# Optimization experiments

Hardware: AMD Instinct MI355X
Metric: run time of the kernel (lower is better)

Reference implementation:

```python
import jax, jax.numpy as jnp
import numpy as np
import math

GROUPS = 32
EPS = 1e-5
N_HEADS = 8  # channels=512 / num_head_channels=64


def group_norm(x, w, b):
    # x: [B, C, T]; GroupNorm over (channels-in-group, T)
    B, C, T = x.shape
    xg = x.reshape(B, GROUPS, C // GROUPS * T)
    mu = xg.mean(axis=-1, keepdims=True)
    var = xg.var(axis=-1, keepdims=True)
    xn = ((xg - mu) * jax.lax.rsqrt(var + EPS)).reshape(B, C, T)
    return xn * w[None, :, None] + b[None, :, None]


def setup_inputs() -> dict:
    key = jax.random.key(0)
    ks = jax.random.split(key, 7)
    C = 512
    return {
        "x": jax.random.normal(ks[0], (8, C, 32, 32), dtype=jnp.float32),
        "norm_w": jax.random.normal(ks[1], (C,), dtype=jnp.float32),
        "norm_b": jax.random.normal(ks[2], (C,), dtype=jnp.float32),
        "qkv_w": jax.random.normal(ks[3], (3 * C, C), dtype=jnp.float32) * 0.02,
        "qkv_b": jax.random.normal(ks[4], (3 * C,), dtype=jnp.float32) * 0.02,
        "proj_w": jax.random.normal(ks[5], (C, C), dtype=jnp.float32) * 0.02,
        "proj_b": jax.random.normal(ks[6], (C,), dtype=jnp.float32) * 0.02,
    }


def reference(x, norm_w, norm_b, qkv_w, qkv_b, proj_w, proj_b):
    b, c, H, W = x.shape
    T = H * W
    xf = x.reshape(b, c, T)
    xn = group_norm(xf, norm_w, norm_b)
    # 1x1 conv1d == channel matmul: [3C, C] x [B, C, T] -> [B, 3C, T]
    qkv = jnp.einsum('oc,bct->bot', qkv_w, xn) + qkv_b[None, :, None]
    ch = c // N_HEADS
    qkv = qkv.reshape(b * N_HEADS, 3 * ch, T)
    q, k, v = qkv[:, :ch], qkv[:, ch:2 * ch], qkv[:, 2 * ch:]
    scale = 1.0 / math.sqrt(math.sqrt(ch))
    # [BH, T, T] score matrix (explicit, as in the original)
    weight = jnp.einsum('bct,bcs->bts', q * scale, k * scale)
    weight = jax.nn.softmax(weight.astype(jnp.float32), axis=-1).astype(qkv.dtype)
    a = jnp.einsum('bts,bcs->bct', weight, v).reshape(b, c, T)
    hout = jnp.einsum('oc,bct->bot', proj_w, a) + proj_b[None, :, None]
    return (xf + hout).reshape(b, c, H, W)
```

## Files before the change

kernel.cpp:

```cpp
#include <hip/hip_runtime.h>
#include <math.h>

typedef float f32x4_t __attribute__((ext_vector_type(4)));
typedef short bf16x8_t __attribute__((ext_vector_type(8)));

#define B_   8
#define C_   512
#define T_   1024
#define NH_  8
#define CH_  64
#define EPSF 1e-5f

#define MFMA16(a, b, c) __builtin_amdgcn_mfma_f32_16x16x32_bf16((a), (b), (c), 0, 0, 0)

__device__ __forceinline__ unsigned short f2bf(float f) {
  union { float f; unsigned u; } v; v.f = f;
  unsigned r = v.u + 0x7FFFu + ((v.u >> 16) & 1u);
  return (unsigned short)(r >> 16);
}

__global__ __launch_bounds__(256) void prep_gn_kernel(
    const float* __restrict__ x, const float* __restrict__ w,
    const float* __restrict__ bvec, unsigned short* __restrict__ xnT,
    const float* __restrict__ qw_f, const float* __restrict__ pw_f,
    unsigned short* __restrict__ qw, unsigned short* __restrict__ pw)
{
  int tid = threadIdx.x;
  if (blockIdx.x >= 256) {
    int idx = (blockIdx.x - 256) * 256 + tid;
    const int N1 = 1536 * 512 / 4;
    const int N2 = 512 * 512 / 4;
    if (idx < N1) {
      float4 v = ((const float4*)qw_f)[idx];
      uint2 o;
      o.x = (unsigned)f2bf(v.x) | ((unsigned)f2bf(v.y) << 16);
      o.y = (unsigned)f2bf(v.z) | ((unsigned)f2bf(v.w) << 16);
      ((uint2*)qw)[idx] = o;
    } else if (idx < N1 + N2) {
      int j = idx - N1;
      float4 v = ((const float4*)pw_f)[j];
      uint2 o;
      o.x = (unsigned)f2bf(v.x) | ((unsigned)f2bf(v.y) << 16);
      o.y = (unsigned)f2bf(v.z) | ((unsigned)f2bf(v.w) << 16);
      ((uint2*)pw)[j] = o;
    }
    return;
  }

  int blk = blockIdx.x;
  int b = blk >> 5, g = blk & 31;
  const float* xp = x + ((size_t)(b * C_ + g * 16)) * T_;
  const int N = 16 * T_;

  float s = 0.f, s2 = 0.f;
  for (int i = tid * 4; i < N; i += 256 * 4) {
    float4 v = *(const float4*)(xp + i);
    s  += v.x + v.y + v.z + v.w;
    s2 += v.x * v.x + v.y * v.y + v.z * v.z + v.w * v.w;
  }
  for (int off = 32; off; off >>= 1) {
    s  += __shfl_down(s,  off, 64);
    s2 += __shfl_down(s2, off, 64);
  }
  __shared__ float rs_[4], r2_[4];
  __shared__ float mu_s, rsig_s;
  int wid = tid >> 6, lane = tid & 63;
  if (lane == 0) { rs_[wid] = s; r2_[wid] = s2; }
  __syncthreads();
  if (tid == 0) {
    float ts = rs_[0] + rs_[1] + rs_[2] + rs_[3];
    float t2 = r2_[0] + r2_[1] + r2_[2] + r2_[3];
    float mu = ts / (float)N;
    float var = t2 / (float)N - mu * mu;
    mu_s = mu;
    rsig_s = rsqrtf(var + EPSF);
  }
  __syncthreads();
  float mu = mu_s, rs = rsig_s;

  float wl[16], bl[16];
  for (int c = 0; c < 16; ++c) { wl[c] = w[g * 16 + c]; bl[c] = bvec[g * 16 + c]; }

  for (int t = tid; t < T_; t += 256) {
    unsigned short buf[16] __attribute__((aligned(16)));
    for (int c = 0; c < 16; ++c) {
      float val = xp[(size_t)c * T_ + t];
      buf[c] = f2bf((val - mu) * rs * wl[c] + bl[c]);
    }
    unsigned short* dst = xnT + ((size_t)b * T_ + t) * C_ + g * 16;
    *(uint4*)dst       = *(uint4*)buf;
    *(uint4*)(dst + 8) = *(uint4*)(buf + 8);
  }
}

__global__ __launch_bounds__(256) void gemm_qkv_kernel(
    const unsigned short* __restrict__ W, const unsigned short* __restrict__ xnT,
    const float* __restrict__ bias,
    unsigned short* __restrict__ q_t, unsigned short* __restrict__ k_t,
    unsigned short* __restrict__ v_c)
{
  int b = blockIdx.z;
  int m0 = blockIdx.y * 128, n0 = blockIdx.x * 128;
  int tid = threadIdx.x;
  int w = tid >> 6, lane = tid & 63, quad = lane >> 4, lr = lane & 15;
  int wm = w >> 1, wn = w & 1;

  __shared__ __align__(16) unsigned short Asl[128][40];
  __shared__ __align__(16) unsigned short Bsl[128][40];

  f32x4_t acc[4][4];
  for (int i = 0; i < 4; ++i)
    for (int j = 0; j < 4; ++j) acc[i][j] = (f32x4_t){0.f, 0.f, 0.f, 0.f};

  const unsigned short* Bbase = xnT + ((size_t)b * T_ + n0) * C_;

  int ur = tid >> 2, uk = (tid & 3) * 8;
  uint4 pa0 = *(const uint4*)&W[(size_t)(m0 + ur) * C_ + uk];
  uint4 pa1 = *(const uint4*)&W[(size_t)(m0 + ur + 64) * C_ + uk];
  uint4 pb0 = *(const uint4*)&Bbase[(size_t)ur * C_ + uk];
  uint4 pb1 = *(const uint4*)&Bbase[(size_t)(ur + 64) * C_ + uk];

  for (int k0 = 0; k0 < C_; k0 += 32) {
    __syncthreads();
    *(uint4*)&Asl[ur][uk]      = pa0;
    *(uint4*)&Asl[ur + 64][uk] = pa1;
    *(uint4*)&Bsl[ur][uk]      = pb0;
    *(uint4*)&Bsl[ur + 64][uk] = pb1;
    if (k0 + 32 < C_) {
      pa0 = *(const uint4*)&W[(size_t)(m0 + ur) * C_ + k0 + 32 + uk];
      pa1 = *(const uint4*)&W[(size_t)(m0 + ur + 64) * C_ + k0 + 32 + uk];
      pb0 = *(const uint4*)&Bbase[(size_t)ur * C_ + k0 + 32 + uk];
      pb1 = *(const uint4*)&Bbase[(size_t)(ur + 64) * C_ + k0 + 32 + uk];
    }
    __syncthreads();
    bf16x8_t af[4], bfv[4];
    for (int i = 0; i < 4; ++i) af[i]  = *(bf16x8_t*)&Asl[wm * 64 + i * 16 + lr][quad * 8];
    for (int j = 0; j < 4; ++j) bfv[j] = *(bf16x8_t*)&Bsl[wn * 64 + j * 16 + lr][quad * 8];
    for (int i = 0; i < 4; ++i)
      for (int j = 0; j < 4; ++j)
        acc[i][j] = MFMA16(af[i], bfv[j], acc[i][j]);
  }

  for (int i = 0; i < 4; ++i) {
    int ob = m0 + wm * 64 + i * 16 + quad * 4;
    int h = ob / 192, r0 = ob % 192;
    for (int j = 0; j < 4; ++j) {
      int t = n0 + wn * 64 + j * 16 + lr;
      if (r0 < 128) {
        unsigned short pk[4] __attribute__((aligned(8)));
      #pragma unroll
        for (int r = 0; r < 4; ++r) pk[r] = f2bf(acc[i][j][r] + bias[ob + r]);
        unsigned short* base = (r0 < 64) ? q_t : k_t;
        int chn = (r0 < 64) ? r0 : r0 - 64;
        *(uint2*)&base[((size_t)(b * NH_ + h) * T_ + t) * CH_ + chn] = *(uint2*)pk;
      } else {
      #pragma unroll
        for (int r = 0; r < 4; ++r) {
          float vv = acc[i][j][r] + bias[ob + r];
          v_c[((size_t)(b * NH_ + h) * CH_ + (r0 - 128 + r)) * T_ + t] = f2bf(vv);
        }
      }
    }
  }
}

__global__ __launch_bounds__(256) void attn_kernel(
    const unsigned short* __restrict__ q_t, const unsigned short* __restrict__ k_t,
    const unsigned short* __restrict__ v_c, unsigned short* __restrict__ a_t)
{
  int t0 = blockIdx.x * 64;
  int bh = blockIdx.y;
  int tid = threadIdx.x;
  int w = tid >> 6, lane = tid & 63, quad = lane >> 4, lr = lane & 15;

  __shared__ __align__(16) unsigned short q_s[64][72];
  __shared__ __align__(16) unsigned short k_s[64][72];
  __shared__ __align__(16) unsigned short v_s[64][72];
  __shared__ __align__(16) unsigned short p_s[64][72];

  int r0 = tid >> 3, c0 = (tid & 7) * 8;
  *(uint4*)&q_s[r0][c0] =
      *(const uint4*)&q_t[((size_t)bh * T_ + t0 + r0) * CH_ + c0];
  *(uint4*)&q_s[r0 + 32][c0] =
      *(const uint4*)&q_t[((size_t)bh * T_ + t0 + r0 + 32) * CH_ + c0];

  uint4 kr0 = *(const uint4*)&k_t[((size_t)bh * T_ + r0) * CH_ + c0];
  uint4 kr1 = *(const uint4*)&k_t[((size_t)bh * T_ + r0 + 32) * CH_ + c0];
  uint4 vr0 = *(const uint4*)&v_c[((size_t)bh * CH_ + r0) * T_ + c0];
  uint4 vr1 = *(const uint4*)&v_c[((size_t)bh * CH_ + r0 + 32) * T_ + c0];

  __syncthreads();
  bf16x8_t aq[2];
  aq[0] = *(bf16x8_t*)&q_s[w * 16 + lr][quad * 8];
  aq[1] = *(bf16x8_t*)&q_s[w * 16 + lr][32 + quad * 8];

  bf16x8_t ones8;
  {
    short ov = (lr == 0) ? (short)0x3F80 : (short)0;
    for (int e = 0; e < 8; ++e) ones8[e] = ov;
  }

  f32x4_t o_acc[4], o_l;
  for (int j = 0; j < 4; ++j) o_acc[j] = (f32x4_t){0.f, 0.f, 0.f, 0.f};
  o_l = (f32x4_t){0.f, 0.f, 0.f, 0.f};

  const float SCL = 0.18033688f;
  const float MSH = 11.541560f;

  for (int s0 = 0; s0 < T_; s0 += 64) {
    __syncthreads();
    *(uint4*)&k_s[r0][c0]      = kr0;
    *(uint4*)&k_s[r0 + 32][c0] = kr1;
    *(uint4*)&v_s[r0][c0]      = vr0;
    *(uint4*)&v_s[r0 + 32][c0] = vr1;
    if (s0 + 64 < T_) {
      kr0 = *(const uint4*)&k_t[((size_t)bh * T_ + s0 + 64 + r0) * CH_ + c0];
      kr1 = *(const uint4*)&k_t[((size_t)bh * T_ + s0 + 96 + r0) * CH_ + c0];
      vr0 = *(const uint4*)&v_c[((size_t)bh * CH_ + r0) * T_ + s0 + 64 + c0];
      vr1 = *(const uint4*)&v_c[((size_t)bh * CH_ + r0 + 32) * T_ + s0 + 64 + c0];
    }
    __syncthreads();

    f32x4_t sc[4];
    for (int j = 0; j < 4; ++j) {
      f32x4_t a2 = (f32x4_t){0.f, 0.f, 0.f, 0.f};
      for (int kk = 0; kk < 2; ++kk) {
        bf16x8_t bk = *(bf16x8_t*)&k_s[j * 16 + lr][kk * 32 + quad * 8];
        a2 = MFMA16(aq[kk], bk, a2);
      }
      sc[j] = a2;
    }

    for (int j = 0; j < 4; ++j)
      for (int r = 0; r < 4; ++r) {
        float p = __builtin_amdgcn_exp2f(sc[j][r] * SCL - MSH);
        union { float f; unsigned u; } cv; cv.f = p;
        p_s[w * 16 + quad * 4 + r][j * 16 + lr] = (unsigned short)(cv.u >> 16);
      }
    bf16x8_t ap[2];
    ap[0] = *(bf16x8_t*)&p_s[w * 16 + lr][quad * 8];
    ap[1] = *(bf16x8_t*)&p_s[w * 16 + lr][32 + quad * 8];

    o_l = MFMA16(ap[0], ones8, o_l);
    o_l = MFMA16(ap[1], ones8, o_l);
    for (int j = 0; j < 4; ++j)
      for (int kk = 0; kk < 2; ++kk) {
        bf16x8_t bv = *(bf16x8_t*)&v_s[j * 16 + lr][kk * 32 + quad * 8];
        o_acc[j] = MFMA16(ap[kk], bv, o_acc[j]);
      }
  }

  float lv[4];
  for (int r = 0; r < 4; ++r) lv[r] = __shfl(o_l[r], lane & 48, 64);
  for (int r = 0; r < 4; ++r) {
    float inv = 1.f / lv[r];
    for (int j = 0; j < 4; ++j)
      q_s[w * 16 + quad * 4 + r][j * 16 + lr] = f2bf(o_acc[j][r] * inv);
  }
  __syncthreads();
  *(uint4*)&a_t[((size_t)bh * T_ + t0 + r0) * CH_ + c0]      = *(uint4*)&q_s[r0][c0];
  *(uint4*)&a_t[((size_t)bh * T_ + t0 + r0 + 32) * CH_ + c0] = *(uint4*)&q_s[r0 + 32][c0];
}

__global__ __launch_bounds__(256) void gemm_proj_kernel(
    const unsigned short* __restrict__ W, const unsigned short* __restrict__ a_t,
    const float* __restrict__ bias, const float* __restrict__ xres,
    float* __restrict__ out)
{
  int b = blockIdx.z;
  int m0 = blockIdx.y * 128, n0 = blockIdx.x * 128;
  int tid = threadIdx.x;
  int w = tid >> 6, lane = tid & 63, quad = lane >> 4, lr = lane & 15;
  int wm = w >> 1, wn = w & 1;

  __shared__ __align__(16) unsigned short Asl[128][40];
  __shared__ __align__(16) unsigned short Bsl[128][40];

  f32x4_t acc[4][4];
  for (int i = 0; i < 4; ++i)
    for (int j = 0; j < 4; ++j) acc[i][j] = (f32x4_t){0.f, 0.f, 0.f, 0.f};

  int ur = tid >> 2, uk = (tid & 3) * 8;
  const unsigned short* Bb0 = a_t + ((size_t)(b * NH_ + 0) * T_ + n0) * CH_;
  uint4 pa0 = *(const uint4*)&W[(size_t)(m0 + ur) * C_ + uk];
  uint4 pa1 = *(const uint4*)&W[(size_t)(m0 + ur + 64) * C_ + uk];
  uint4 pb0 = *(const uint4*)&Bb0[(size_t)ur * CH_ + uk];
  uint4 pb1 = *(const uint4*)&Bb0[(size_t)(ur + 64) * CH_ + uk];

  for (int k0 = 0; k0 < C_; k0 += 32) {
    __syncthreads();
    *(uint4*)&Asl[ur][uk]      = pa0;
    *(uint4*)&Asl[ur + 64][uk] = pa1;
    *(uint4*)&Bsl[ur][uk]      = pb0;
    *(uint4*)&Bsl[ur + 64][uk] = pb1;
    if (k0 + 32 < C_) {
      int kn = k0 + 32;
      const unsigned short* Bb =
          a_t + ((size_t)(b * NH_ + (kn >> 6)) * T_ + n0) * CH_ + (kn & 63);
      pa0 = *(const uint4*)&W[(size_t)(m0 + ur) * C_ + kn + uk];
      pa1 = *(const uint4*)&W[(size_t)(m0 + ur + 64) * C_ + kn + uk];
      pb0 = *(const uint4*)&Bb[(size_t)ur * CH_ + uk];
      pb1 = *(const uint4*)&Bb[(size_t)(ur + 64) * CH_ + uk];
    }
    __syncthreads();
    bf16x8_t af[4], bfv[4];
    for (int i = 0; i < 4; ++i) af[i]  = *(bf16x8_t*)&Asl[wm * 64 + i * 16 + lr][quad * 8];
    for (int j = 0; j < 4; ++j) bfv[j] = *(bf16x8_t*)&Bsl[wn * 64 + j * 16 + lr][quad * 8];
    for (int i = 0; i < 4; ++i)
      for (int j = 0; j < 4; ++j)
        acc[i][j] = MFMA16(af[i], bfv[j], acc[i][j]);
  }

  for (int i = 0; i < 4; ++i) {
    int ob = m0 + wm * 64 + i * 16 + quad * 4;
    for (int j = 0; j < 4; ++j) {
      int t = n0 + wn * 64 + j * 16 + lr;
    #pragma unroll
      for (int r = 0; r < 4; ++r) {
        size_t idx = ((size_t)(b * C_ + ob + r)) * T_ + t;
        out[idx] = acc[i][j][r] + bias[ob + r] + xres[idx];
      }
    }
  }
}

extern "C" void kernel_launch(void* const* d_in, const int* in_sizes, int n_in,
                              void* d_out, int out_size, void* d_ws, size_t ws_size,
                              hipStream_t stream)
{
  const float* x      = (const float*)d_in[0];
  const float* norm_w = (const float*)d_in[1];
  const float* norm_b = (const float*)d_in[2];
  const float* qkv_w  = (const float*)d_in[3];
  const float* qkv_b  = (const float*)d_in[4];
  const float* proj_w = (const float*)d_in[5];
  const float* proj_b = (const float*)d_in[6];
  float* out = (float*)d_out;

  char* ws = (char*)d_ws;
  unsigned short* qw  = (unsigned short*)ws;
  unsigned short* pw  = (unsigned short*)(ws + 1572864);
  unsigned short* xnT = (unsigned short*)(ws + 2097152);
  unsigned short* q_t = (unsigned short*)(ws + 10485760);
  unsigned short* k_t = (unsigned short*)(ws + 18874368);
  unsigned short* v_c = (unsigned short*)(ws + 27262976);
  unsigned short* a_t = (unsigned short*)(ws + 35651584);

  prep_gn_kernel<<<dim3(256 + 1024), dim3(256), 0, stream>>>(
      x, norm_w, norm_b, xnT, qkv_w, proj_w, qw, pw);

  gemm_qkv_kernel<<<dim3(T_ / 128, 1536 / 128, B_), dim3(256), 0, stream>>>(
      qw, xnT, qkv_b, q_t, k_t, v_c);

  attn_kernel<<<dim3(T_ / 64, B_ * NH_), dim3(256), 0, stream>>>(q_t, k_t, v_c, a_t);

  gemm_proj_kernel<<<dim3(T_ / 128, C_ / 128, B_), dim3(256), 0, stream>>>(
      pw, a_t, proj_b, x, out);
}
```

Before: 165.8 us.

## Restructure attention kernel to keep P in registers with transposed MFMA

The attention kernel now computes S^T = K·Q^T so the exponentiated scores land in registers in the layout needed as the B operand of the PV MFMA. This removes the p_s shared-memory round trip. Each wave now handles 64 query rows instead of 16, so every K/V tile loaded into LDS is reused across four times as many queries, with 2 waves per block and a permuted K row layout in LDS. The cost is much higher register pressure from 16 score and 16 output accumulator tiles per wave, plus fewer blocks in flight (512 instead of 1024).

```diff
diff --git a/kernel.cpp b/kernel.cpp
--- a/kernel.cpp
+++ b/kernel.cpp
@@ -17,6 +17,15 @@
   union { float f; unsigned u; } v; v.f = f;
   unsigned r = v.u + 0x7FFFu + ((v.u >> 16) & 1u);
   return (unsigned short)(r >> 16);
+}
+
+__device__ __forceinline__ unsigned pkbf(float lo, float hi) {
+  union { float f; unsigned u; } a, b; a.f = lo; b.f = hi;
+#if __has_builtin(__builtin_amdgcn_perm)
+  return __builtin_amdgcn_perm(b.u, a.u, 0x07060302u);
+#else
+  return (a.u >> 16) | (b.u & 0xFFFF0000u);
+#endif
 }
 
 __global__ __launch_bounds__(256) void prep_gn_kernel(
@@ -164,102 +173,136 @@
   }
 }
 
-__global__ __launch_bounds__(256) void attn_kernel(
+__global__ __launch_bounds__(128, 2) void attn_kernel(
     const unsigned short* __restrict__ q_t, const unsigned short* __restrict__ k_t,
     const unsigned short* __restrict__ v_c, unsigned short* __restrict__ a_t)
 {
-  int t0 = blockIdx.x * 64;
+  int t0 = blockIdx.x * 128;
   int bh = blockIdx.y;
   int tid = threadIdx.x;
   int w = tid >> 6, lane = tid & 63, quad = lane >> 4, lr = lane & 15;
 
-  __shared__ __align__(16) unsigned short q_s[64][72];
   __shared__ __align__(16) unsigned short k_s[64][72];
   __shared__ __align__(16) unsigned short v_s[64][72];
-  __shared__ __align__(16) unsigned short p_s[64][72];
-
-  int r0 = tid >> 3, c0 = (tid & 7) * 8;
-  *(uint4*)&q_s[r0][c0] =
-      *(const uint4*)&q_t[((size_t)bh * T_ + t0 + r0) * CH_ + c0];
-  *(uint4*)&q_s[r0 + 32][c0] =
-      *(const uint4*)&q_t[((size_t)bh * T_ + t0 + r0 + 32) * CH_ + c0];
-
-  uint4 kr0 = *(const uint4*)&k_t[((size_t)bh * T_ + r0) * CH_ + c0];
-  uint4 kr1 = *(const uint4*)&k_t[((size_t)bh * T_ + r0 + 32) * CH_ + c0];
-  uint4 vr0 = *(const uint4*)&v_c[((size_t)bh * CH_ + r0) * T_ + c0];
-  uint4 vr1 = *(const uint4*)&v_c[((size_t)bh * CH_ + r0 + 32) * T_ + c0];
-
-  __syncthreads();
-  bf16x8_t aq[2];
-  aq[0] = *(bf16x8_t*)&q_s[w * 16 + lr][quad * 8];
-  aq[1] = *(bf16x8_t*)&q_s[w * 16 + lr][32 + quad * 8];
-
-  bf16x8_t ones8;
+
+  const unsigned short* qb = q_t + (size_t)bh * T_ * CH_;
+  const unsigned short* kb = k_t + (size_t)bh * T_ * CH_;
+  const unsigned short* vb = v_c + (size_t)bh * CH_ * T_;
+
+  int tw = t0 + w * 64;
+  bf16x8_t aq[4][2];
+  for (int tf = 0; tf < 4; ++tf)
+    for (int kk = 0; kk < 2; ++kk)
+      aq[tf][kk] = *(const bf16x8_t*)
+          &qb[(size_t)(tw + tf * 16 + lr) * CH_ + kk * 32 + quad * 8];
+
+  uint4 kr[4], vr[4];
+  for (int u = 0; u < 4; ++u) {
+    int idx = u * 128 + tid;
+    int row = idx >> 3, c8 = (idx & 7) * 8;
+    kr[u] = *(const uint4*)&kb[(size_t)row * CH_ + c8];
+    vr[u] = *(const uint4*)&vb[(size_t)row * T_ + c8];
+  }
+
+  bf16x8_t onesA;
   {
     short ov = (lr == 0) ? (short)0x3F80 : (short)0;
-    for (int e = 0; e < 8; ++e) ones8[e] = ov;
-  }
-
-  f32x4_t o_acc[4], o_l;
-  for (int j = 0; j < 4; ++j) o_acc[j] = (f32x4_t){0.f, 0.f, 0.f, 0.f};
-  o_l = (f32x4_t){0.f, 0.f, 0.f, 0.f};
+    for (int e = 0; e < 8; ++e) onesA[e] = ov;
+  }
+
+  f32x4_t o_acc[4][4];
+  f32x4_t o_l[4];
+  for (int i = 0; i < 4; ++i) {
+    o_l[i] = (f32x4_t){0.f, 0.f, 0.f, 0.f};
+    for (int j = 0; j < 4; ++j) o_acc[i][j] = (f32x4_t){0.f, 0.f, 0.f, 0.f};
+  }
 
   const float SCL = 0.18033688f;
   const float MSH = 11.541560f;
 
   for (int s0 = 0; s0 < T_; s0 += 64) {
+    if (s0) __syncthreads();
+    for (int u = 0; u < 4; ++u) {
+      int idx = u * 128 + tid;
+      int row = idx >> 3, c8 = (idx & 7) * 8;
+      int gr = (row & 0x23) | ((row & 4) << 2) | ((row & 0x18) >> 1);
+      *(uint4*)&k_s[gr][c8]  = kr[u];
+      *(uint4*)&v_s[row][c8] = vr[u];
+    }
+    if (s0 + 64 < T_) {
+      for (int u = 0; u < 4; ++u) {
+        int idx = u * 128 + tid;
+        int row = idx >> 3, c8 = (idx & 7) * 8;
+        kr[u] = *(const uint4*)&kb[(size_t)(s0 + 64 + row) * CH_ + c8];
+        vr[u] = *(const uint4*)&vb[(size_t)row * T_ + s0 + 64 + c8];
+      }
+    }
     __syncthreads();
-    *(uint4*)&k_s[r0][c0]      = kr0;
-    *(uint4*)&k_s[r0 + 32][c0] = kr1;
-    *(uint4*)&v_s[r0][c0]      = vr0;
-    *(uint4*)&v_s[r0 + 32][c0] = vr1;
-    if (s0 + 64 < T_) {
-      kr0 = *(const uint4*)&k_t[((size_t)bh * T_ + s0 + 64 + r0) * CH_ + c0];
-      kr1 = *(const uint4*)&k_t[((size_t)bh * T_ + s0 + 96 + r0) * CH_ + c0];
-      vr0 = *(const uint4*)&v_c[((size_t)bh * CH_ + r0) * T_ + s0 + 64 + c0];
-      vr1 = *(const uint4*)&v_c[((size_t)bh * CH_ + r0 + 32) * T_ + s0 + 64 + c0];
-    }
-    __syncthreads();
-
-    f32x4_t sc[4];
-    for (int j = 0; j < 4; ++j) {
-      f32x4_t a2 = (f32x4_t){0.f, 0.f, 0.f, 0.f};
-      for (int kk = 0; kk < 2; ++kk) {
-        bf16x8_t bk = *(bf16x8_t*)&k_s[j * 16 + lr][kk * 32 + quad * 8];
-        a2 = MFMA16(aq[kk], bk, a2);
+
+    f32x4_t sc[4][4];
+    for (int mt = 0; mt < 4; ++mt)
+      for (int tf = 0; tf < 4; ++tf) sc[mt][tf] = (f32x4_t){0.f, 0.f, 0.f, 0.f};
+    for (int kk = 0; kk < 2; ++kk) {
+      bf16x8_t kf[4];
+      for (int mt = 0; mt < 4; ++mt)
+        kf[mt] = *(const bf16x8_t*)&k_s[mt * 16 + lr][kk * 32 + quad * 8];
+      for (int mt = 0; mt < 4; ++mt)
+        for (int tf = 0; tf < 4; ++tf)
+          sc[mt][tf] = MFMA16(kf[mt], aq[tf][kk], sc[mt][tf]);
+    }
+
+    unsigned pk[4][4][2];
+    for (int mt = 0; mt < 4; ++mt)
+      for (int tf = 0; tf < 4; ++tf) {
+        float p0 = __builtin_amdgcn_exp2f(sc[mt][tf][0] * SCL - MSH);
+        float p1 = __builtin_amdgcn_exp2f(sc[mt][tf][1] * SCL - MSH);
+        float p2 = __builtin_amdgcn_exp2f(sc[mt][tf][2] * SCL - MSH);
+        float p3 = __builtin_amdgcn_exp2f(sc[mt][tf][3] * SCL - MSH);
+        pk[mt][tf][0] = pkbf(p0, p1);
+        pk[mt][tf][1] = pkbf(p2, p3);
       }
-      sc[j] = a2;
-    }
-
-    for (int j = 0; j < 4; ++j)
-      for (int r = 0; r < 4; ++r) {
-        float p = __builtin_amdgcn_exp2f(sc[j][r] * SCL - MSH);
-        union { float f; unsigned u; } cv; cv.f = p;
-        p_s[w * 16 + quad * 4 + r][j * 16 + lr] = (unsigned short)(cv.u >> 16);
+
+    for (int kk = 0; kk < 2; ++kk) {
+      bf16x8_t vf[4];
+      for (int cht = 0; cht < 4; ++cht)
+        vf[cht] = *(const bf16x8_t*)&v_s[cht * 16 + lr][kk * 32 + quad * 8];
+      for (int tf = 0; tf < 4; ++tf) {
+        union { unsigned u[4]; bf16x8_t v; } bp;
+        bp.u[0] = pk[2 * kk][tf][0];
+        bp.u[1] = pk[2 * kk][tf][1];
+        bp.u[2] = pk[2 * kk + 1][tf][0];
+        bp.u[3] = pk[2 * kk + 1][tf][1];
+        o_l[tf] = MFMA16(onesA, bp.v, o_l[tf]);
+        for (int cht = 0; cht < 4; ++cht)
+          o_acc[cht][tf] = MFMA16(vf[cht], bp.v, o_acc[cht][tf]);
       }
-    bf16x8_t ap[2];
-    ap[0] = *(bf16x8_t*)&p_s[w * 16 + lr][quad * 8];
-    ap[1] = *(bf16x8_t*)&p_s[w * 16 + lr][32 + quad * 8];
-
-    o_l = MFMA16(ap[0], ones8, o_l);
-    o_l = MFMA16(ap[1], ones8, o_l);
-    for (int j = 0; j < 4; ++j)
-      for (int kk = 0; kk < 2; ++kk) {
-        bf16x8_t bv = *(bf16x8_t*)&v_s[j * 16 + lr][kk * 32 + quad * 8];
-        o_acc[j] = MFMA16(ap[kk], bv, o_acc[j]);
-      }
-  }
-
-  float lv[4];
-  for (int r = 0; r < 4; ++r) lv[r] = __shfl(o_l[r], lane & 48, 64);
-  for (int r = 0; r < 4; ++r) {
-    float inv = 1.f / lv[r];
-    for (int j = 0; j < 4; ++j)
-      q_s[w * 16 + quad * 4 + r][j * 16 + lr] = f2bf(o_acc[j][r] * inv);
-  }
+    }
+  }
+
   __syncthreads();
-  *(uint4*)&a_t[((size_t)bh * T_ + t0 + r0) * CH_ + c0]      = *(uint4*)&q_s[r0][c0];
-  *(uint4*)&a_t[((size_t)bh * T_ + t0 + r0 + 32) * CH_ + c0] = *(uint4*)&q_s[r0 + 32][c0];
+  float inv_[4];
+  for (int tf = 0; tf < 4; ++tf) {
+    float lv = __shfl(o_l[tf][0], lane & 15, 64);
+    inv_[tf] = 1.f / lv;
+  }
+  unsigned short (*ob)[72] = w ? v_s : k_s;
+  for (int cht = 0; cht < 4; ++cht)
+    for (int tf = 0; tf < 4; ++tf) {
+      float inv = inv_[tf];
+      f32x4_t o = o_acc[cht][tf];
+      uint2 pr;
+      pr.x = pkbf(o[0] * inv, o[1] * inv);
+      pr.y = pkbf(o[2] * inv, o[3] * inv);
+      *(uint2*)&ob[tf * 16 + lr][cht * 16 + quad * 4] = pr;
+    }
+  __syncthreads();
+  for (int u = 0; u < 8; ++u) {
+    int idx = u * 128 + tid;
+    int tl = idx >> 3, c8 = (idx & 7) * 8;
+    const unsigned short (*sb)[72] = (tl < 64) ? k_s : v_s;
+    *(uint4*)&a_t[((size_t)bh * T_ + t0 + tl) * CH_ + c8] =
+        *(const uint4*)&sb[tl & 63][c8];
+  }
 }
 
 __global__ __launch_bounds__(256) void gemm_proj_kernel(
@@ -352,7 +395,7 @@
   gemm_qkv_kernel<<<dim3(T_ / 128, 1536 / 128, B_), dim3(256), 0, stream>>>(
       qw, xnT, qkv_b, q_t, k_t, v_c);
 
-  attn_kernel<<<dim3(T_ / 64, B_ * NH_), dim3(256), 0, stream>>>(q_t, k_t, v_c, a_t);
+  attn_kernel<<<dim3(T_ / 128, B_ * NH_), dim3(128), 0, stream>>>(q_t, k_t, v_c, a_t);
 
   gemm_proj_kernel<<<dim3(T_ / 128, C_ / 128, B_), dim3(256), 0, stream>>>(
       pw, a_t, proj_b, x, out);
```

Measured after the change: 188.4 us. +13.6%, slower.
